# Optimization experiments

Hardware: AMD Instinct MI355X
Metric: run time of the kernel (lower is better)

The kernel has to match this reference:

```python
import jax, jax.numpy as jnp
import numpy as np

B, C, H, W = 4, 64, 96, 96
HEAD_SIZE = 4


def setup_inputs() -> dict:
    key = jax.random.key(0)
    ks = jax.random.split(key, 9)
    s = 1.0 / np.sqrt(C)
    d = {"x": jax.random.normal(ks[0], (B, C, H, W), dtype=jnp.float32)}
    for i, name in enumerate(["Wq", "Wk", "Wv", "Wo"]):
        d[name] = jax.random.normal(ks[1 + i], (C, C), dtype=jnp.float32) * s
    for i, name in enumerate(["bq", "bk", "bv", "bo"]):
        d[name] = jax.random.normal(ks[5 + i], (C,), dtype=jnp.float32) * 0.01
    return d


def reference(x, Wq, bq, Wk, bk, Wv, bv, Wo, bo):
    b, c, h, w = x.shape
    hw = h * w
    hs = HEAD_SIZE
    S = hw // hs  # spatial tokens per head (heads split along HW, not channels)
    scale = 1.0 / jnp.sqrt(jnp.asarray(hs, x.dtype))

    def proj(y, Wm, bias):  # 1x1 conv == per-pixel channel matmul
        return jnp.einsum('bchw,oc->bohw', y, Wm) + bias[None, :, None, None]

    def heads(y):  # (B,C,H,W) -> (B,hs,C,S)
        return y.reshape(b, c, hs, S).transpose(0, 2, 1, 3)

    q = heads(proj(x, Wq, bq))  # (B,hs,C,S)
    k = heads(proj(x, Wk, bk))  # (B,hs,C,S)
    v = heads(proj(x, Wv, bv))  # (B,hs,C,S)

    # attention = softmax(q^T k / sqrt(head_size)) over last axis: (B,hs,S,S)
    attn = jax.nn.softmax(jnp.einsum('bhcs,bhct->bhst', q, k) * scale, axis=-1)
    # out = v @ attn^T : (B,hs,C,S)
    out = jnp.einsum('bhcs,bhts->bhct', v, attn)
    # torch .reshape on the (B,hs,C,S) layout -> (B,C,H,W); jnp.reshape matches
    out = out.reshape(b, c, h, w)
    out = jnp.einsum('bchw,oc->bohw', out, Wo) + bo[None, :, None, None]
    return x + out
```

## Files before the change

### kernel.cpp

```cpp
#include <hip/hip_runtime.h>
#include <stdint.h>

#define HW_  9216
#define S_   2304
#define NBH  16
#define NSPLIT 3
#define JPS  12
#define NPART ((size_t)NBH * S_ * 64)
#define SCALE_LOG2E 0.72134752044448169136f

using f32x4 = __attribute__((ext_vector_type(4))) float;
using u32x4 = __attribute__((ext_vector_type(4))) uint32_t;
using u32x2 = __attribute__((ext_vector_type(2))) uint32_t;
using s16x8 = __attribute__((ext_vector_type(8))) short;

typedef const __attribute__((address_space(1))) void gbl_void;
typedef __attribute__((address_space(3))) void lds_void;

__device__ __forceinline__ uint32_t pkbf(float lo, float hi) {
    uint32_t r;
    asm("v_cvt_pk_bf16_f32 %0, %1, %2" : "=v"(r) : "v"(lo), "v"(hi));
    return r;
}
__device__ __forceinline__ float bf2f(uint16_t h) {
    return __builtin_bit_cast(float, (uint32_t)h << 16);
}

__global__ __launch_bounds__(64) void qkv_proj(
    const float* __restrict__ x,
    const float* __restrict__ Wq, const float* __restrict__ Wk, const float* __restrict__ Wv,
    const float* __restrict__ bq, const float* __restrict__ bk, const float* __restrict__ bv,
    uint16_t* __restrict__ Qo, uint16_t* __restrict__ Ko, uint16_t* __restrict__ Vo)
{
    const int mode = blockIdx.y;
    const float* W    = (mode == 0) ? Wq : (mode == 1) ? Wk : Wv;
    const float* bias = (mode == 0) ? bq : (mode == 1) ? bk : bv;
    const float ws = (mode == 0) ? SCALE_LOG2E : 1.0f;

    const int pix0 = blockIdx.x * 64;
    const int b   = pix0 / HW_;
    const int hw0 = pix0 % HW_;
    const int h   = hw0 / S_;
    const int s0  = hw0 % S_;
    const int bh  = b * 4 + h;

    const int lane = threadIdx.x;
    const int g = lane >> 4, lr = lane & 15;

    __shared__ alignas(16) uint16_t xt[64 * 64];

    {
        const float* xb = x + (size_t)b * 64 * HW_ + hw0 + lane;
        uint32_t rp[32];
        #pragma unroll
        for (int cc = 0; cc < 32; ++cc)
            rp[cc] = pkbf(xb[(size_t)(2 * cc) * HW_], xb[(size_t)(2 * cc + 1) * HW_]);
        #pragma unroll
        for (int cb = 0; cb < 8; ++cb) {
            u32x4 d = { rp[cb * 4], rp[cb * 4 + 1], rp[cb * 4 + 2], rp[cb * 4 + 3] };
            *(u32x4*)(xt + lane * 64 + 8 * (cb ^ (lane & 7))) = d;
        }
    }
    __syncthreads();

    s16x8 wf[4][2];
    #pragma unroll
    for (int t4 = 0; t4 < 4; ++t4)
        #pragma unroll
        for (int ks = 0; ks < 2; ++ks) {
            const float* wp = W + (t4 * 16 + lr) * 64 + ks * 32 + g * 8;
            f32x4 w0 = *(const f32x4*)wp;
            f32x4 w1 = *(const f32x4*)(wp + 4);
            u32x4 d = { pkbf(w0[0] * ws, w0[1] * ws), pkbf(w0[2] * ws, w0[3] * ws),
                        pkbf(w1[0] * ws, w1[1] * ws), pkbf(w1[2] * ws, w1[3] * ws) };
            wf[t4][ks] = __builtin_bit_cast(s16x8, d);
        }

    s16x8 xf[4][2];
    #pragma unroll
    for (int pt = 0; pt < 4; ++pt)
        #pragma unroll
        for (int ks = 0; ks < 2; ++ks) {
            const int pix = pt * 16 + lr;
            xf[pt][ks] = *(const s16x8*)(xt + pix * 64 + 8 * ((ks * 4 + g) ^ (pix & 7)));
        }

    f32x4 acc[4][4];
    if (mode != 2) {
        #pragma unroll
        for (int mt = 0; mt < 4; ++mt) {
            f32x4 bi = *(const f32x4*)(bias + mt * 16 + g * 4);
            bi *= ws;
            #pragma unroll
            for (int nt = 0; nt < 4; ++nt) acc[mt][nt] = bi;
        }
        #pragma unroll
        for (int ks = 0; ks < 2; ++ks)
            #pragma unroll
            for (int mt = 0; mt < 4; ++mt)
                #pragma unroll
                for (int nt = 0; nt < 4; ++nt)
                    acc[mt][nt] = __builtin_amdgcn_mfma_f32_16x16x32_bf16(
                        wf[mt][ks], xf[nt][ks], acc[mt][nt], 0, 0, 0);
        uint16_t* dst = ((mode == 0) ? Qo : Ko) + ((size_t)bh * S_ + s0) * 64;
        #pragma unroll
        for (int mt = 0; mt < 4; ++mt)
            #pragma unroll
            for (int nt = 0; nt < 4; ++nt) {
                uint32_t d0 = pkbf(acc[mt][nt][0], acc[mt][nt][1]);
                uint32_t d1 = pkbf(acc[mt][nt][2], acc[mt][nt][3]);
                const int o = mt * 16 + g * 4;
                *(uint32_t*)(dst + (nt * 16 + lr) * 64 + o)     = d0;
                *(uint32_t*)(dst + (nt * 16 + lr) * 64 + o + 2) = d1;
            }
    } else {
        #pragma unroll
        for (int nt = 0; nt < 4; ++nt) {
            const float bv = bias[nt * 16 + lr];
            #pragma unroll
            for (int mt = 0; mt < 4; ++mt) acc[mt][nt] = (f32x4){bv, bv, bv, bv};
        }
        #pragma unroll
        for (int ks = 0; ks < 2; ++ks)
            #pragma unroll
            for (int mt = 0; mt < 4; ++mt)
                #pragma unroll
                for (int nt = 0; nt < 4; ++nt)
                    acc[mt][nt] = __builtin_amdgcn_mfma_f32_16x16x32_bf16(
                        xf[mt][ks], wf[nt][ks], acc[mt][nt], 0, 0, 0);
        uint16_t* dst = Vo + (size_t)bh * 64 * S_;
        #pragma unroll
        for (int mt = 0; mt < 4; ++mt)
            #pragma unroll
            for (int nt = 0; nt < 4; ++nt) {
                uint32_t d0 = pkbf(acc[mt][nt][0], acc[mt][nt][1]);
                uint32_t d1 = pkbf(acc[mt][nt][2], acc[mt][nt][3]);
                const int o = nt * 16 + lr;
                const int sb = s0 + mt * 16 + g * 4;
                *(uint32_t*)(dst + (size_t)o * S_ + sb)     = d0;
                *(uint32_t*)(dst + (size_t)o * S_ + sb + 2) = d1;
            }
    }
}

__global__ __launch_bounds__(256, 3) void attn(
    const uint16_t* __restrict__ Qg, const uint16_t* __restrict__ Kg,
    const uint16_t* __restrict__ Vg, uint16_t* __restrict__ Op,
    float* __restrict__ Lp)
{
    const int blk = blockIdx.x;
    const int xcd = blk & 7;
    const int i   = blk >> 3;
    const int bh  = xcd * 2 + (i & 1);
    const int i2  = i >> 1;
    const int sp  = i2 % 3;
    const int qb  = i2 / 3;
    const int j0  = sp * JPS;
    const int b   = bh >> 2;
    const int h   = bh & 3;

    const int tid  = threadIdx.x;
    const int wave = tid >> 6;
    const int lane = tid & 63;
    const int g    = lane >> 4;
    const int lr   = lane & 15;
    const int q0   = qb * 128 + wave * 32;

    __shared__ alignas(16) uint16_t Kl[4096];
    __shared__ alignas(16) uint16_t Vl[4096];
    __shared__ alignas(16) uint16_t Pw[4][2304];
    uint16_t* P = Pw[wave];

    const uint16_t* Qb = Qg + (size_t)bh * S_ * 64;
    const uint16_t* Kb = Kg + (size_t)bh * S_ * 64;
    const uint16_t* Vb = Vg + (size_t)bh * 64 * S_;

    s16x8 qf[2][2];
    #pragma unroll
    for (int qt = 0; qt < 2; ++qt)
        #pragma unroll
        for (int ks = 0; ks < 2; ++ks)
            qf[qt][ks] = *(const s16x8*)(Qb + (size_t)(q0 + qt * 16 + lr) * 64 + ks * 32 + g * 8);

    f32x4 oacc[2][4];
    float l_r[2][4];
    #pragma unroll
    for (int qt = 0; qt < 2; ++qt) {
        #pragma unroll
        for (int ct = 0; ct < 4; ++ct) oacc[qt][ct] = (f32x4){0.f, 0.f, 0.f, 0.f};
        #pragma unroll
        for (int r = 0; r < 4; ++r) l_r[qt][r] = 0.f;
    }

    for (int jj = 0; jj < JPS; ++jj) {
        const int j = j0 + jj;
        #pragma unroll
        for (int call = 0; call < 2; ++call) {
            const int chunk = wave * 128 + call * 64 + lane;
            const int row   = chunk >> 3;
            const int cb    = (chunk & 7) ^ (row & 7);
            __builtin_amdgcn_global_load_lds(
                (gbl_void*)(Kb + ((size_t)(j * 64 + row) * 64 + cb * 8)),
                (lds_void*)(Kl + (wave * 128 + call * 64) * 8), 16, 0, 0);
            __builtin_amdgcn_global_load_lds(
                (gbl_void*)(Vb + ((size_t)row * S_ + j * 64 + cb * 8)),
                (lds_void*)(Vl + (wave * 128 + call * 64) * 8), 16, 0, 0);
        }
        asm volatile("s_waitcnt vmcnt(0)" ::: "memory");
        __syncthreads();

        f32x4 sacc[2][4];
        #pragma unroll
        for (int qt = 0; qt < 2; ++qt)
            #pragma unroll
            for (int kt = 0; kt < 4; ++kt) sacc[qt][kt] = (f32x4){0.f, 0.f, 0.f, 0.f};
        #pragma unroll
        for (int ks = 0; ks < 2; ++ks)
            #pragma unroll
            for (int kt = 0; kt < 4; ++kt) {
                const int key = kt * 16 + lr;
                s16x8 kf = *(const s16x8*)(&Kl[key * 64 + 8 * ((ks * 4 + g) ^ (key & 7))]);
                sacc[0][kt] = __builtin_amdgcn_mfma_f32_16x16x32_bf16(qf[0][ks], kf, sacc[0][kt], 0, 0, 0);
                sacc[1][kt] = __builtin_amdgcn_mfma_f32_16x16x32_bf16(qf[1][ks], kf, sacc[1][kt], 0, 0, 0);
            }

        #pragma unroll
        for (int qt = 0; qt < 2; ++qt)
            #pragma unroll
            for (int kt = 0; kt < 4; ++kt)
                #pragma unroll
                for (int r = 0; r < 4; ++r) {
                    const float pv = __builtin_amdgcn_exp2f(sacc[qt][kt][r]);
                    l_r[qt][r] += pv;
                    P[(qt * 16 + 4 * g + r) * 72 + kt * 16 + lr] = (uint16_t)pkbf(pv, pv);
                }

        #pragma unroll
        for (int ks = 0; ks < 2; ++ks) {
            s16x8 pf0 = *(const s16x8*)(P + (0 * 16 + lr) * 72 + ks * 32 + g * 8);
            s16x8 pf1 = *(const s16x8*)(P + (1 * 16 + lr) * 72 + ks * 32 + g * 8);
            #pragma unroll
            for (int ct = 0; ct < 4; ++ct) {
                const int c = ct * 16 + lr;
                s16x8 vf = *(const s16x8*)(&Vl[c * 64 + 8 * ((ks * 4 + g) ^ (c & 7))]);
                oacc[0][ct] = __builtin_amdgcn_mfma_f32_16x16x32_bf16(pf0, vf, oacc[0][ct], 0, 0, 0);
                oacc[1][ct] = __builtin_amdgcn_mfma_f32_16x16x32_bf16(pf1, vf, oacc[1][ct], 0, 0, 0);
            }
        }

        __syncthreads();
    }

    #pragma unroll
    for (int mask = 1; mask < 16; mask <<= 1) {
        #pragma unroll
        for (int qt = 0; qt < 2; ++qt)
            #pragma unroll
            for (int r = 0; r < 4; ++r)
                l_r[qt][r] += __shfl_xor(l_r[qt][r], mask, 64);
    }

    #pragma unroll
    for (int qt = 0; qt < 2; ++qt)
        #pragma unroll
        for (int ct = 0; ct < 4; ++ct) {
            uint32_t d0 = pkbf(oacc[qt][ct][0], oacc[qt][ct][1]);
            uint32_t d1 = pkbf(oacc[qt][ct][2], oacc[qt][ct][3]);
            const int base = (ct * 16 + lr) * 36 + qt * 16 + 4 * g;
            *(uint32_t*)(P + base)     = d0;
            *(uint32_t*)(P + base + 2) = d1;
        }
    __syncthreads();

    const int c = lane;
    u32x2 wv[8];
    #pragma unroll
    for (int e = 0; e < 8; ++e)
        wv[e] = *(const u32x2*)(P + c * 36 + e * 4);
    uint16_t* dst = Op + (size_t)sp * NPART
                  + ((size_t)(b * 64 + h * 16 + (c >> 2)) * HW_ + (c & 3) * S_ + q0);
    #pragma unroll
    for (int s4 = 0; s4 < 4; ++s4) {
        u32x4 d = { wv[2 * s4][0], wv[2 * s4][1], wv[2 * s4 + 1][0], wv[2 * s4 + 1][1] };
        *(u32x4*)(dst + s4 * 8) = d;
    }

    if (lr == 0) {
        #pragma unroll
        for (int qt = 0; qt < 2; ++qt)
            #pragma unroll
            for (int r = 0; r < 4; ++r)
                Lp[((size_t)sp * NBH + bh) * S_ + q0 + qt * 16 + 4 * g + r] = l_r[qt][r];
    }
}

__global__ __launch_bounds__(64) void out_proj(
    const uint16_t* __restrict__ Op, const float* __restrict__ Lp,
    const float* __restrict__ x,
    const float* __restrict__ Wo, const float* __restrict__ bo,
    float* __restrict__ out)
{
    const int pix0 = blockIdx.x * 64;
    const int b   = pix0 / HW_;
    const int hw0 = pix0 % HW_;
    const int lane = threadIdx.x;
    const int g = lane >> 4, lr = lane & 15;
    const int t = (hw0 % S_) + lane;

    __shared__ alignas(16) uint16_t at[64 * 64];

    float inv[4];
    #pragma unroll
    for (int hh = 0; hh < 4; ++hh) {
        float sl = 0.f;
        #pragma unroll
        for (int sp2 = 0; sp2 < NSPLIT; ++sp2)
            sl += Lp[((size_t)sp2 * NBH + b * 4 + hh) * S_ + t];
        inv[hh] = 1.0f / sl;
    }

    {
        const size_t base = (size_t)b * 64 * HW_ + hw0 + lane;
        uint32_t rp[32];
        #pragma unroll
        for (int cc = 0; cc < 32; ++cc) {
            float a0 = 0.f, a1 = 0.f;
            #pragma unroll
            for (int sp2 = 0; sp2 < NSPLIT; ++sp2) {
                const size_t o2 = (size_t)sp2 * NPART + base;
                a0 += bf2f(Op[o2 + (size_t)(2 * cc) * HW_]);
                a1 += bf2f(Op[o2 + (size_t)(2 * cc + 1) * HW_]);
            }
            rp[cc] = pkbf(a0 * inv[(2 * cc) >> 4], a1 * inv[(2 * cc + 1) >> 4]);
        }
        #pragma unroll
        for (int cb = 0; cb < 8; ++cb) {
            u32x4 d = { rp[cb * 4], rp[cb * 4 + 1], rp[cb * 4 + 2], rp[cb * 4 + 3] };
            *(u32x4*)(at + lane * 64 + 8 * (cb ^ (lane & 7))) = d;
        }
    }
    __syncthreads();

    s16x8 wf[4][2];
    #pragma unroll
    for (int t4 = 0; t4 < 4; ++t4)
        #pragma unroll
        for (int ks = 0; ks < 2; ++ks) {
            const float* wp = Wo + (t4 * 16 + lr) * 64 + ks * 32 + g * 8;
            f32x4 w0 = *(const f32x4*)wp;
            f32x4 w1 = *(const f32x4*)(wp + 4);
            u32x4 d = { pkbf(w0[0], w0[1]), pkbf(w0[2], w0[3]),
                        pkbf(w1[0], w1[1]), pkbf(w1[2], w1[3]) };
            wf[t4][ks] = __builtin_bit_cast(s16x8, d);
        }

    s16x8 af[4][2];
    #pragma unroll
    for (int pt = 0; pt < 4; ++pt)
        #pragma unroll
        for (int ks = 0; ks < 2; ++ks) {
            const int pix = pt * 16 + lr;
            af[pt][ks] = *(const s16x8*)(at + pix * 64 + 8 * ((ks * 4 + g) ^ (pix & 7)));
        }

    f32x4 acc[4][4];
    #pragma unroll
    for (int mt = 0; mt < 4; ++mt) {
        f32x4 bi = *(const f32x4*)(bo + mt * 16 + g * 4);
        #pragma unroll
        for (int nt = 0; nt < 4; ++nt) acc[mt][nt] = bi;
    }
    #pragma unroll
    for (int ks = 0; ks < 2; ++ks)
        #pragma unroll
        for (int mt = 0; mt < 4; ++mt)
            #pragma unroll
            for (int nt = 0; nt < 4; ++nt)
                acc[mt][nt] = __builtin_amdgcn_mfma_f32_16x16x32_bf16(
                    wf[mt][ks], af[nt][ks], acc[mt][nt], 0, 0, 0);

    #pragma unroll
    for (int mt = 0; mt < 4; ++mt)
        #pragma unroll
        for (int nt = 0; nt < 4; ++nt) {
            const int o = mt * 16 + g * 4;
            const size_t rowb = ((size_t)(b * 64 + o)) * HW_ + hw0 + nt * 16 + lr;
            #pragma unroll
            for (int r = 0; r < 4; ++r) {
                const size_t a2 = rowb + (size_t)r * HW_;
                out[a2] = acc[mt][nt][r] + x[a2];
            }
        }
}

extern "C" void kernel_launch(void* const* d_in, const int* in_sizes, int n_in,
                              void* d_out, int out_size, void* d_ws, size_t ws_size,
                              hipStream_t stream) {
    const float* x  = (const float*)d_in[0];
    const float* Wq = (const float*)d_in[1];
    const float* Wk = (const float*)d_in[2];
    const float* Wv = (const float*)d_in[3];
    const float* Wo = (const float*)d_in[4];
    const float* bq = (const float*)d_in[5];
    const float* bk = (const float*)d_in[6];
    const float* bv = (const float*)d_in[7];
    const float* bo = (const float*)d_in[8];
    float* out = (float*)d_out;

    uint16_t* Q  = (uint16_t*)d_ws;
    uint16_t* K  = Q + NPART;
    uint16_t* V  = K + NPART;
    uint16_t* Op = V + NPART;
    float*    Lp = (float*)(Op + (size_t)NSPLIT * NPART);

    qkv_proj<<<dim3(576, 3), 64, 0, stream>>>(x, Wq, Wk, Wv, bq, bk, bv, Q, K, V);
    attn<<<864, 256, 0, stream>>>(Q, K, V, Op, Lp);
    out_proj<<<576, 64, 0, stream>>>(Op, Lp, x, Wo, bo, out);
}
```

Before: 68.85 us.

## Fuse QKV projection into one block, raise KV split to four, split out_proj channels

```diff
diff --git a/kernel.cpp b/kernel.cpp
--- a/kernel.cpp
+++ b/kernel.cpp
@@ -4,8 +4,8 @@
 #define HW_  9216
 #define S_   2304
 #define NBH  16
-#define NSPLIT 3
-#define JPS  12
+#define NSPLIT 4
+#define JPS  9
 #define NPART ((size_t)NBH * S_ * 64)
 #define SCALE_LOG2E 0.72134752044448169136f
 
@@ -26,17 +26,12 @@
     return __builtin_bit_cast(float, (uint32_t)h << 16);
 }
 
-__global__ __launch_bounds__(64) void qkv_proj(
+__global__ __launch_bounds__(192) void qkv_fused(
     const float* __restrict__ x,
     const float* __restrict__ Wq, const float* __restrict__ Wk, const float* __restrict__ Wv,
     const float* __restrict__ bq, const float* __restrict__ bk, const float* __restrict__ bv,
     uint16_t* __restrict__ Qo, uint16_t* __restrict__ Ko, uint16_t* __restrict__ Vo)
 {
-    const int mode = blockIdx.y;
-    const float* W    = (mode == 0) ? Wq : (mode == 1) ? Wk : Wv;
-    const float* bias = (mode == 0) ? bq : (mode == 1) ? bk : bv;
-    const float ws = (mode == 0) ? SCALE_LOG2E : 1.0f;
-
     const int pix0 = blockIdx.x * 64;
     const int b   = pix0 / HW_;
     const int hw0 = pix0 % HW_;
@@ -44,24 +39,32 @@
     const int s0  = hw0 % S_;
     const int bh  = b * 4 + h;
 
-    const int lane = threadIdx.x;
+    const int tid  = threadIdx.x;
+    const int wave = tid >> 6;
+    const int lane = tid & 63;
     const int g = lane >> 4, lr = lane & 15;
 
     __shared__ alignas(16) uint16_t xt[64 * 64];
 
     {
         const float* xb = x + (size_t)b * 64 * HW_ + hw0 + lane;
-        uint32_t rp[32];
-        #pragma unroll
-        for (int cc = 0; cc < 32; ++cc)
-            rp[cc] = pkbf(xb[(size_t)(2 * cc) * HW_], xb[(size_t)(2 * cc + 1) * HW_]);
-        #pragma unroll
-        for (int cb = 0; cb < 8; ++cb) {
-            u32x4 d = { rp[cb * 4], rp[cb * 4 + 1], rp[cb * 4 + 2], rp[cb * 4 + 3] };
+        const int cb_begin = wave * 3;
+        const int cb_end   = (wave == 2) ? 8 : wave * 3 + 3;
+        for (int cb = cb_begin; cb < cb_end; ++cb) {
+            uint32_t rp[4];
+            #pragma unroll
+            for (int e = 0; e < 4; ++e)
+                rp[e] = pkbf(xb[(size_t)(cb * 8 + 2 * e) * HW_],
+                             xb[(size_t)(cb * 8 + 2 * e + 1) * HW_]);
+            u32x4 d = { rp[0], rp[1], rp[2], rp[3] };
             *(u32x4*)(xt + lane * 64 + 8 * (cb ^ (lane & 7))) = d;
         }
     }
     __syncthreads();
+
+    const float* W    = (wave == 0) ? Wq : (wave == 1) ? Wk : Wv;
+    const float* bias = (wave == 0) ? bq : (wave == 1) ? bk : bv;
+    const float ws = (wave == 0) ? SCALE_LOG2E : 1.0f;
 
     s16x8 wf[4][2];
     #pragma unroll
@@ -85,8 +88,8 @@
             xf[pt][ks] = *(const s16x8*)(xt + pix * 64 + 8 * ((ks * 4 + g) ^ (pix & 7)));
         }
 
-    f32x4 acc[4][4];
-    if (mode != 2) {
+    if (wave != 2) {
+        f32x4 acc[4][4];
         #pragma unroll
         for (int mt = 0; mt < 4; ++mt) {
             f32x4 bi = *(const f32x4*)(bias + mt * 16 + g * 4);
@@ -102,7 +105,7 @@
                 for (int nt = 0; nt < 4; ++nt)
                     acc[mt][nt] = __builtin_amdgcn_mfma_f32_16x16x32_bf16(
                         wf[mt][ks], xf[nt][ks], acc[mt][nt], 0, 0, 0);
-        uint16_t* dst = ((mode == 0) ? Qo : Ko) + ((size_t)bh * S_ + s0) * 64;
+        uint16_t* dst = ((wave == 0) ? Qo : Ko) + ((size_t)bh * S_ + s0) * 64;
         #pragma unroll
         for (int mt = 0; mt < 4; ++mt)
             #pragma unroll
@@ -114,6 +117,7 @@
                 *(uint32_t*)(dst + (nt * 16 + lr) * 64 + o + 2) = d1;
             }
     } else {
+        f32x4 acc[4][4];
         #pragma unroll
         for (int nt = 0; nt < 4; ++nt) {
             const float bv = bias[nt * 16 + lr];
@@ -153,8 +157,8 @@
     const int i   = blk >> 3;
     const int bh  = xcd * 2 + (i & 1);
     const int i2  = i >> 1;
-    const int sp  = i2 % 3;
-    const int qb  = i2 / 3;
+    const int sp  = i2 & 3;
+    const int qb  = i2 >> 2;
     const int j0  = sp * JPS;
     const int b   = bh >> 2;
     const int h   = bh & 3;
@@ -301,6 +305,7 @@
     float* __restrict__ out)
 {
     const int pix0 = blockIdx.x * 64;
+    const int o0   = blockIdx.y * 32;
     const int b   = pix0 / HW_;
     const int hw0 = pix0 % HW_;
     const int lane = threadIdx.x;
@@ -341,17 +346,17 @@
     }
     __syncthreads();
 
-    s16x8 wf[4][2];
-    #pragma unroll
-    for (int t4 = 0; t4 < 4; ++t4)
+    s16x8 wf[2][2];
+    #pragma unroll
+    for (int t2 = 0; t2 < 2; ++t2)
         #pragma unroll
         for (int ks = 0; ks < 2; ++ks) {
-            const float* wp = Wo + (t4 * 16 + lr) * 64 + ks * 32 + g * 8;
+            const float* wp = Wo + (o0 + t2 * 16 + lr) * 64 + ks * 32 + g * 8;
             f32x4 w0 = *(const f32x4*)wp;
             f32x4 w1 = *(const f32x4*)(wp + 4);
             u32x4 d = { pkbf(w0[0], w0[1]), pkbf(w0[2], w0[3]),
                         pkbf(w1[0], w1[1]), pkbf(w1[2], w1[3]) };
-            wf[t4][ks] = __builtin_bit_cast(s16x8, d);
+            wf[t2][ks] = __builtin_bit_cast(s16x8, d);
         }
 
     s16x8 af[4][2];
@@ -363,27 +368,27 @@
             af[pt][ks] = *(const s16x8*)(at + pix * 64 + 8 * ((ks * 4 + g) ^ (pix & 7)));
         }
 
-    f32x4 acc[4][4];
-    #pragma unroll
-    for (int mt = 0; mt < 4; ++mt) {
-        f32x4 bi = *(const f32x4*)(bo + mt * 16 + g * 4);
+    f32x4 acc[2][4];
+    #pragma unroll
+    for (int mt = 0; mt < 2; ++mt) {
+        f32x4 bi = *(const f32x4*)(bo + o0 + mt * 16 + g * 4);
         #pragma unroll
         for (int nt = 0; nt < 4; ++nt) acc[mt][nt] = bi;
     }
     #pragma unroll
     for (int ks = 0; ks < 2; ++ks)
         #pragma unroll
-        for (int mt = 0; mt < 4; ++mt)
+        for (int mt = 0; mt < 2; ++mt)
             #pragma unroll
             for (int nt = 0; nt < 4; ++nt)
                 acc[mt][nt] = __builtin_amdgcn_mfma_f32_16x16x32_bf16(
                     wf[mt][ks], af[nt][ks], acc[mt][nt], 0, 0, 0);
 
     #pragma unroll
-    for (int mt = 0; mt < 4; ++mt)
+    for (int mt = 0; mt < 2; ++mt)
         #pragma unroll
         for (int nt = 0; nt < 4; ++nt) {
-            const int o = mt * 16 + g * 4;
+            const int o = o0 + mt * 16 + g * 4;
             const size_t rowb = ((size_t)(b * 64 + o)) * HW_ + hw0 + nt * 16 + lr;
             #pragma unroll
             for (int r = 0; r < 4; ++r) {
@@ -413,7 +418,7 @@
     uint16_t* Op = V + NPART;
     float*    Lp = (float*)(Op + (size_t)NSPLIT * NPART);
 
-    qkv_proj<<<dim3(576, 3), 64, 0, stream>>>(x, Wq, Wk, Wv, bq, bk, bv, Q, K, V);
-    attn<<<864, 256, 0, stream>>>(Q, K, V, Op, Lp);
-    out_proj<<<576, 64, 0, stream>>>(Op, Lp, x, Wo, bo, out);
-}
+    qkv_fused<<<576, 192, 0, stream>>>(x, Wq, Wk, Wv, bq, bk, bv, Q, K, V);
+    attn<<<1152, 256, 0, stream>>>(Q, K, V, Op, Lp);
+    out_proj<<<dim3(576, 2), 64, 0, stream>>>(Op, Lp, x, Wo, bo, out);
+}
```

New measurement: 68.54 us. No clear change (-0.5%).
